# Kernel tuning notes

Hardware: AMD Instinct MI355X
Metric: run time of the kernel (lower is better)

## Reference

```python
import jax, jax.numpy as jnp
import numpy as np

RADIUS = 1.0
NSAMPLE = 32

B, S, C_IN, C_OUT, K = 2, 8192, 64, 64, 15


def setup_inputs() -> dict:
    key = jax.random.key(0)
    k1, k2, k3, k4 = jax.random.split(key, 4)
    query_xyz = jax.random.normal(k1, (B, S, 3), dtype=jnp.float32)
    features = jax.random.normal(k2, (B, S, C_IN), dtype=jnp.float32)
    weights = jax.random.normal(k3, (K, C_IN, C_OUT), dtype=jnp.float32) * 0.005
    kp = jax.random.normal(k4, (K, 3), dtype=jnp.float32)
    kp = kp / jnp.linalg.norm(kp, axis=1, keepdims=True) * RADIUS
    kp = kp.at[0].set(jnp.zeros(3, dtype=jnp.float32))  # fixed center point
    return {"query_xyz": query_xyz, "features": features,
            "weights": weights, "kernel_points": kp}


def _square_distance(src, dst):
    # (B,N,3),(B,M,3) -> (B,N,M)
    d = -2.0 * jnp.einsum('bnc,bmc->bnm', src, dst)
    d += jnp.sum(src ** 2, axis=-1, keepdims=True)
    d += jnp.sum(dst ** 2, axis=-1)[:, None, :]
    return d


def reference(query_xyz, features, weights, kernel_points):
    # ball query (self-query: xyz == new_xyz)
    sqrdists = _square_distance(query_xyz, query_xyz)          # (B,S,S)
    idx = jnp.argsort(sqrdists, axis=-1)[:, :, :NSAMPLE]        # (B,S,ns)
    grouped_dists = jnp.take_along_axis(sqrdists, idx, axis=2)
    mask = grouped_dists > RADIUS ** 2
    idx = jnp.where(mask, idx[:, :, :1], idx)

    # gather neighbor features and coordinates: (B,S,ns,C), (B,S,ns,3)
    grouped_features = jnp.take_along_axis(features[:, None, :, :], idx[..., None], axis=2)
    grouped_xyz = jnp.take_along_axis(query_xyz[:, None, :, :], idx[..., None], axis=2)
    relative_xyz = grouped_xyz - query_xyz[:, :, None, :]       # (B,S,ns,3)

    # squared distance to each kernel point: (B,S,ns,K)
    diff = relative_xyz[:, :, :, None, :] - kernel_points[None, None, None, :, :]
    sq_dist = jnp.maximum(jnp.sum(diff ** 2, axis=-1), 0.0)

    # linear influence
    influence = jnp.maximum(1.0 - jnp.sqrt(sq_dist + 1e-8) / (RADIUS + 1e-8), 0.0)

    # fused weight-aggregate (same math as expand+multiply+sum in the original)
    agg = jnp.einsum('bsnk,bsnc->bskc', influence, grouped_features)  # (B,S,K,C_in)
    out = jnp.einsum('bskc,kco->bso', agg, weights)                    # (B,S,C_out)
    return (query_xyz, out)
```

## Files before the change

### kernel.cpp

```cpp
#include <hip/hip_runtime.h>

#define B_    2
#define S_    8192
#define CIN_  64
#define COUT_ 64
#define K_    15
#define NS_   32

typedef unsigned long long u64;
typedef unsigned int u32;
typedef unsigned short u16;
typedef __attribute__((ext_vector_type(8))) short short8;
typedef __attribute__((ext_vector_type(4))) float f32x4;

union U4S8 { uint4 u; short8 s; };

__device__ __forceinline__ u32 f2bf(float x){
  u32 u = __float_as_uint(x);
  return (u + 0x7FFFu + ((u >> 16) & 1u)) >> 16;
}

__device__ __forceinline__ void cx(u64 &k, int j, bool up, int lane){
  u64 o = __shfl_xor(k, j, 64);
  bool lower = (lane & j) == 0;
  bool take = (up == lower) ? (o < k) : (o > k);
  if (take) k = o;
}
__device__ __forceinline__ void sort64(u64 &k, int lane){
  #pragma unroll
  for (int kk = 2; kk <= 64; kk <<= 1){
    #pragma unroll
    for (int j = kk >> 1; j > 0; j >>= 1) cx(k, j, (lane & kk) == 0, lane);
  }
}
__device__ __forceinline__ void merge32(u64 &k, int lane){
  #pragma unroll
  for (int j = 16; j > 0; j >>= 1) cx(k, j, true, lane);
}

__global__ __launch_bounds__(256) void kp_select(const float* __restrict__ xyz,
                                                 int* __restrict__ nbr){
  __shared__ u64 buf[4][2][128];

  const int tid = threadIdx.x, w = tid >> 6, lane = tid & 63;
  const int qbase = blockIdx.x * 8 + w * 2;
  const int b = qbase >> 13;
  const float* base = xyz + (size_t)b * S_ * 3;

  float qx[2], qy[2], qz[2], sqq[2];
  #pragma unroll
  for (int i = 0; i < 2; ++i){
    int s = (qbase + i) & (S_ - 1);
    qx[i] = base[s*3]; qy[i] = base[s*3+1]; qz[i] = base[s*3+2];
    sqq[i] = qx[i]*qx[i] + qy[i]*qy[i] + qz[i]*qz[i];
  }

  u64 rkey[2] = {~0ull, ~0ull};
  u32 kmd[2]  = {0xBF800000u, 0xBF800000u};
  int cnt[2]  = {0, 0};

  float cxv = base[lane*3], cyv = base[lane*3+1], czv = base[lane*3+2];

  for (int ch = 0; ch < 128; ++ch){
    float nxv = cxv, nyv = cyv, nzv = czv;
    if (ch < 127){
      int p = (ch + 1) * 64 + lane;
      nxv = base[p*3]; nyv = base[p*3+1]; nzv = base[p*3+2];
    }
    float sqp = cxv*cxv + cyv*cyv + czv*czv;
    int pidx = ch * 64 + lane;
    #pragma unroll
    for (int i = 0; i < 2; ++i){
      float dot = qx[i]*cxv + qy[i]*cyv + qz[i]*czv;
      float d = -2.0f * dot; d = d + sqq[i]; d = d + sqp;
      u32 md = __float_as_uint(d);
      md ^= (u32)((int)md >> 31) | 0x80000000u;
      bool pred = md <= kmd[i];
      u64 m = __ballot(pred);
      if (m){
        int pos = cnt[i] + (int)__popcll(m & ((1ull << lane) - 1ull));
        if (pred) buf[w][i][pos] = ((u64)md << 13) | (u32)pidx;
        cnt[i] += (int)__popcll(m);
        if (cnt[i] >= 64){
          cnt[i] -= 64;
          asm volatile("s_waitcnt lgkmcnt(0)" ::: "memory");
          u64 ck = buf[w][i][cnt[i] + lane];
          sort64(ck, lane);
          u64 rev = __shfl(ck, (31 - lane) & 63, 64);
          if (rev < rkey[i]) rkey[i] = rev;
          merge32(rkey[i], lane);
          u64 k31 = __shfl(rkey[i], 31, 64);
          kmd[i] = (u32)(k31 >> 13);
        }
      }
    }
    cxv = nxv; cyv = nyv; czv = nzv;
  }

  #pragma unroll
  for (int i = 0; i < 2; ++i){
    if (cnt[i] > 0){
      asm volatile("s_waitcnt lgkmcnt(0)" ::: "memory");
      u64 ck = (lane < cnt[i]) ? buf[w][i][lane] : ~0ull;
      sort64(ck, lane);
      u64 rev = __shfl(ck, (31 - lane) & 63, 64);
      if (rev < rkey[i]) rkey[i] = rev;
      merge32(rkey[i], lane);
    }
    u32 md  = (u32)(rkey[i] >> 13);
    int idx = (int)(rkey[i] & 8191u);
    int i0  = __shfl(idx, 0, 64);
    int wi  = (md > 0xBF800000u) ? i0 : idx;
    if (lane < NS_) nbr[(size_t)(qbase + i) * NS_ + lane] = wi;
  }
}

__global__ void w_cvt(const float* __restrict__ w, u16* __restrict__ wb){
  int idx = blockIdx.x * 256 + threadIdx.x;
  int i    = idx & 7;
  int lane = (idx >> 3) & 63;
  int st   = (idx >> 9) & 31;
  int wo   = idx >> 14;
  int kc   = st * 32 + (lane >> 4) * 8 + i;
  int k    = kc & 15, c = kc >> 4;
  int o    = wo * 16 + (lane & 15);
  float v  = (k < K_) ? w[(k * 64 + c) * 64 + o] : 0.0f;
  wb[idx] = (u16)f2bf(v);
}

__global__ __launch_bounds__(256) void kp_gather(
    const float* __restrict__ xyz, const float* __restrict__ feat,
    const float* __restrict__ kp, const u16* __restrict__ wb,
    const int* __restrict__ nbr, float* __restrict__ outp){
  __shared__ u32 aggA[16 * 512];

  const int tid = threadIdx.x, w = tid >> 6, lane = tid & 63;
  const int qbase = blockIdx.x * 16;
  const int b = qbase >> 13;
  const float* bx = xyz + (size_t)b * S_ * 3;
  const float* fb = feat + (size_t)b * S_ * CIN_;

  const int kk = lane & 15;
  float kx = 0.f, ky = 0.f, kz = 0.f;
  if (kk < 15){ kx = kp[kk*3]; ky = kp[kk*3+1]; kz = kp[kk*3+2]; }

  float agg0[15], agg1[15];

  auto do_q = [&](int ql, float (&agg)[15]){
    const int q = qbase + ql;
    const int s = q & (S_ - 1);
    const float qx = bx[s*3], qy = bx[s*3+1], qz = bx[s*3+2];
    int nl = 0; float nx = 0.f, ny = 0.f, nz = 0.f;
    if (lane < NS_){
      nl = nbr[(size_t)q * NS_ + lane];
      nx = bx[nl*3]; ny = bx[nl*3+1]; nz = bx[nl*3+2];
    }
    const float rx = nx - qx, ry = ny - qy, rz = nz - qz;

    float infl[8];
    #pragma unroll
    for (int jg = 0; jg < 8; ++jg){
      int jj = jg * 4 + (lane >> 4);
      float ax = __shfl(rx, jj, 64), ay = __shfl(ry, jj, 64), az = __shfl(rz, jj, 64);
      float dx = ax - kx, dy = ay - ky, dz = az - kz;
      float sq = dx*dx + dy*dy + dz*dz;
      sq = fmaxf(sq, 0.0f);
      infl[jg] = fmaxf(1.0f - sqrtf(sq + 1e-8f), 0.0f);
    }
    #pragma unroll
    for (int k = 0; k < 15; ++k) agg[k] = 0.0f;
    #pragma unroll
    for (int jg = 0; jg < 8; ++jg){
      int n0 = __shfl(nl, jg*4+0, 64); float f0 = fb[(size_t)n0 * CIN_ + lane];
      int n1 = __shfl(nl, jg*4+1, 64); float f1 = fb[(size_t)n1 * CIN_ + lane];
      int n2 = __shfl(nl, jg*4+2, 64); float f2 = fb[(size_t)n2 * CIN_ + lane];
      int n3 = __shfl(nl, jg*4+3, 64); float f3 = fb[(size_t)n3 * CIN_ + lane];
      u32 iv = __float_as_uint(infl[jg]);
      #pragma unroll
      for (int k = 0; k < 15; ++k){
        float s0 = __uint_as_float(__builtin_amdgcn_readlane(iv, k));
        float s1 = __uint_as_float(__builtin_amdgcn_readlane(iv, 16 + k));
        float s2 = __uint_as_float(__builtin_amdgcn_readlane(iv, 32 + k));
        float s3 = __uint_as_float(__builtin_amdgcn_readlane(iv, 48 + k));
        agg[k] = fmaf(s0, f0, agg[k]);
        agg[k] = fmaf(s1, f1, agg[k]);
        agg[k] = fmaf(s2, f2, agg[k]);
        agg[k] = fmaf(s3, f3, agg[k]);
      }
    }
  };

  auto store_row = [&](int r, float (&agg)[15]){
    u32 pd[8];
    #pragma unroll
    for (int j = 0; j < 7; ++j) pd[j] = (f2bf(agg[2*j+1]) << 16) | f2bf(agg[2*j]);
    pd[7] = f2bf(agg[14]);
    u32* rp = aggA + r * 512;
    int g0 = (lane * 2)     ^ r;
    int g1 = (lane * 2 + 1) ^ r;
    uint4 v0; v0.x = pd[0]; v0.y = pd[1]; v0.z = pd[2]; v0.w = pd[3];
    uint4 v1; v1.x = pd[4]; v1.y = pd[5]; v1.z = pd[6]; v1.w = pd[7];
    *(uint4*)(rp + g0 * 4) = v0;
    *(uint4*)(rp + g1 * 4) = v1;
  };

  #pragma unroll
  for (int pair = 0; pair < 2; ++pair){
    do_q(w * 4 + pair * 2 + 0, agg0);
    do_q(w * 4 + pair * 2 + 1, agg1);
    store_row(w * 4 + pair * 2 + 0, agg0);
    store_row(w * 4 + pair * 2 + 1, agg1);
  }
  __syncthreads();

  const int r  = lane & 15;
  const int kb = lane >> 4;
  f32x4 acc = {0.f, 0.f, 0.f, 0.f};
  const uint4* wb4 = (const uint4*)wb + (size_t)(w * 32) * 64 + lane;
  u32* rp = aggA + r * 512;
  #pragma unroll
  for (int st = 0; st < 32; ++st){
    int gp = (st * 4 + kb) ^ r;
    U4S8 a; a.u = *(const uint4*)(rp + gp * 4);
    U4S8 bfr; bfr.u = wb4[st * 64];
    acc = __builtin_amdgcn_mfma_f32_16x16x32_bf16(a.s, bfr.s, acc, 0, 0, 0);
  }
  #pragma unroll
  for (int j = 0; j < 4; ++j){
    int row = kb * 4 + j;
    outp[(size_t)(qbase + row) * COUT_ + w * 16 + r] = acc[j];
  }
}

extern "C" void kernel_launch(void* const* d_in, const int* in_sizes, int n_in,
                              void* d_out, int out_size, void* d_ws, size_t ws_size,
                              hipStream_t stream) {
  const float* xyz  = (const float*)d_in[0];
  const float* feat = (const float*)d_in[1];
  const float* w    = (const float*)d_in[2];
  const float* kp   = (const float*)d_in[3];

  float* out = (float*)d_out;
  u16*   wb  = (u16*)d_ws;
  int*   nbr = (int*)((char*)d_ws + 131072);

  hipMemcpyAsync(out, xyz, (size_t)B_ * S_ * 3 * sizeof(float),
                 hipMemcpyDeviceToDevice, stream);

  w_cvt<<<256, 256, 0, stream>>>(w, wb);
  kp_select<<<(B_ * S_) / 8, 256, 0, stream>>>(xyz, nbr);
  kp_gather<<<(B_ * S_) / 16, 256, 0, stream>>>(xyz, feat, kp, wb, nbr,
                                                out + (size_t)B_ * S_ * 3);
}
```

Before: 232.5 us.

## Double gather block to 512 threads, split MFMA K-reduction, prefetch features

The gather kernel now runs 8 waves per block, so each wave handles 2 queries instead of 4 and keeps only one aggregate array live. The MFMA projection is split across two wave halves along the reduction dimension, with the partial sums combined through shared memory. Feature loads for the next neighbour group are software-prefetched one iteration ahead. The aim is more parallelism and latency hiding in the gather stage, at the cost of an extra barrier and a shared-memory reduction.

```diff
diff --git a/kernel.cpp b/kernel.cpp
--- a/kernel.cpp
+++ b/kernel.cpp
@@ -128,11 +128,12 @@
   wb[idx] = (u16)f2bf(v);
 }
 
-__global__ __launch_bounds__(256) void kp_gather(
+__global__ __launch_bounds__(512, 7) void kp_gather(
     const float* __restrict__ xyz, const float* __restrict__ feat,
     const float* __restrict__ kp, const u16* __restrict__ wb,
     const int* __restrict__ nbr, float* __restrict__ outp){
   __shared__ u32 aggA[16 * 512];
+  __shared__ float red[4 * 64 * 4];
 
   const int tid = threadIdx.x, w = tid >> 6, lane = tid & 63;
   const int qbase = blockIdx.x * 16;
@@ -144,9 +145,9 @@
   float kx = 0.f, ky = 0.f, kz = 0.f;
   if (kk < 15){ kx = kp[kk*3]; ky = kp[kk*3+1]; kz = kp[kk*3+2]; }
 
-  float agg0[15], agg1[15];
-
-  auto do_q = [&](int ql, float (&agg)[15]){
+  float agg[15];
+
+  auto do_q = [&](int ql){
     const int q = qbase + ql;
     const int s = q & (S_ - 1);
     const float qx = bx[s*3], qy = bx[s*3+1], qz = bx[s*3+2];
@@ -169,12 +170,22 @@
     }
     #pragma unroll
     for (int k = 0; k < 15; ++k) agg[k] = 0.0f;
+
+    int   nn[4]; float ff[4];
+    #pragma unroll
+    for (int t = 0; t < 4; ++t) nn[t] = __shfl(nl, t, 64);
+    #pragma unroll
+    for (int t = 0; t < 4; ++t) ff[t] = fb[(size_t)nn[t] * CIN_ + lane];
+
     #pragma unroll
     for (int jg = 0; jg < 8; ++jg){
-      int n0 = __shfl(nl, jg*4+0, 64); float f0 = fb[(size_t)n0 * CIN_ + lane];
-      int n1 = __shfl(nl, jg*4+1, 64); float f1 = fb[(size_t)n1 * CIN_ + lane];
-      int n2 = __shfl(nl, jg*4+2, 64); float f2 = fb[(size_t)n2 * CIN_ + lane];
-      int n3 = __shfl(nl, jg*4+3, 64); float f3 = fb[(size_t)n3 * CIN_ + lane];
+      float f0 = ff[0], f1 = ff[1], f2 = ff[2], f3 = ff[3];
+      if (jg < 7){
+        #pragma unroll
+        for (int t = 0; t < 4; ++t) nn[t] = __shfl(nl, (jg + 1) * 4 + t, 64);
+        #pragma unroll
+        for (int t = 0; t < 4; ++t) ff[t] = fb[(size_t)nn[t] * CIN_ + lane];
+      }
       u32 iv = __float_as_uint(infl[jg]);
       #pragma unroll
       for (int k = 0; k < 15; ++k){
@@ -190,7 +201,7 @@
     }
   };
 
-  auto store_row = [&](int r, float (&agg)[15]){
+  auto store_row = [&](int r){
     u32 pd[8];
     #pragma unroll
     for (int j = 0; j < 7; ++j) pd[j] = (f2bf(agg[2*j+1]) << 16) | f2bf(agg[2*j]);
@@ -204,31 +215,33 @@
     *(uint4*)(rp + g1 * 4) = v1;
   };
 
-  #pragma unroll
-  for (int pair = 0; pair < 2; ++pair){
-    do_q(w * 4 + pair * 2 + 0, agg0);
-    do_q(w * 4 + pair * 2 + 1, agg1);
-    store_row(w * 4 + pair * 2 + 0, agg0);
-    store_row(w * 4 + pair * 2 + 1, agg1);
-  }
+  do_q(w * 2 + 0); store_row(w * 2 + 0);
+  do_q(w * 2 + 1); store_row(w * 2 + 1);
   __syncthreads();
 
   const int r  = lane & 15;
   const int kb = lane >> 4;
+  const int ob = w & 3, kh = w >> 2;
   f32x4 acc = {0.f, 0.f, 0.f, 0.f};
-  const uint4* wb4 = (const uint4*)wb + (size_t)(w * 32) * 64 + lane;
+  const uint4* wb4 = (const uint4*)wb + (size_t)(ob * 32 + kh * 16) * 64 + lane;
   u32* rp = aggA + r * 512;
   #pragma unroll
-  for (int st = 0; st < 32; ++st){
+  for (int sp = 0; sp < 16; ++sp){
+    int st = kh * 16 + sp;
     int gp = (st * 4 + kb) ^ r;
     U4S8 a; a.u = *(const uint4*)(rp + gp * 4);
-    U4S8 bfr; bfr.u = wb4[st * 64];
+    U4S8 bfr; bfr.u = wb4[sp * 64];
     acc = __builtin_amdgcn_mfma_f32_16x16x32_bf16(a.s, bfr.s, acc, 0, 0, 0);
   }
-  #pragma unroll
-  for (int j = 0; j < 4; ++j){
-    int row = kb * 4 + j;
-    outp[(size_t)(qbase + row) * COUT_ + w * 16 + r] = acc[j];
+  if (kh == 1) *(f32x4*)&red[(ob * 64 + lane) * 4] = acc;
+  __syncthreads();
+  if (kh == 0){
+    const float4 p = *(const float4*)&red[(ob * 64 + lane) * 4];
+    #pragma unroll
+    for (int j = 0; j < 4; ++j){
+      int row = kb * 4 + j;
+      outp[(size_t)(qbase + row) * COUT_ + ob * 16 + r] = acc[j] + (&p.x)[j];
+    }
   }
 }
 
@@ -249,6 +262,6 @@
 
   w_cvt<<<256, 256, 0, stream>>>(w, wb);
   kp_select<<<(B_ * S_) / 8, 256, 0, stream>>>(xyz, nbr);
-  kp_gather<<<(B_ * S_) / 16, 256, 0, stream>>>(xyz, feat, kp, wb, nbr,
+  kp_gather<<<(B_ * S_) / 16, 512, 0, stream>>>(xyz, feat, kp, wb, nbr,
                                                 out + (size_t)B_ * S_ * 3);
 }
```

Measured after the change: 189.9 us. -18.3%, faster.
